# Kernel tuning notes

Measured on AMD Instinct MI355X. Metric: run time of the kernel, lower is better.

## Reference

```python
import jax, jax.numpy as jnp
import numpy as np

D = 4       # number of TT dimensions
N = 128     # mode size per dimension (Ns)
R = 16      # TT rank (RMAX)
B = 262144  # batch of query points


def setup_inputs() -> dict:
    key = jax.random.key(0)
    ks = jax.random.split(key, 5)
    # points in [-1, 1] (remap_needed=True assumes this domain)
    x = jax.random.uniform(ks[0], (B, D), dtype=jnp.float32) * 2.0 - 1.0
    core0 = jax.random.normal(ks[1], (1, N, R), dtype=jnp.float32)
    core1 = jax.random.normal(ks[2], (R, N, R), dtype=jnp.float32)
    core2 = jax.random.normal(ks[3], (R, N, R), dtype=jnp.float32)
    core3 = jax.random.normal(ks[4], (R, N, 1), dtype=jnp.float32)
    return {"x": x, "core0": core0, "core1": core1, "core2": core2, "core3": core3}


def _forward(x, cores):
    # remap: (x + 1) / 2 * (Ns[0] - 1)  (module uses Ns[0] for all dims)
    n0 = cores[0].shape[1]
    xr = (x + 1.0) * 0.5 * (n0 - 1)
    # per-dim clamp to [0, Ns[i]-1]
    ns = jnp.array([c.shape[1] for c in cores], dtype=x.dtype)  # [D]
    xc = jnp.clip(xr, 0.0, ns - 1.0)  # broadcast over D
    idx_low = jnp.floor(xc).astype(jnp.int32)   # [B, D]
    idx_high = jnp.ceil(xc).astype(jnp.int32)   # [B, D]
    wh = xc - idx_low.astype(x.dtype)           # [B, D] interpolation weights
    # gather + linear interpolation per core -> list of [r_prev, B, r_next]
    newcores = []
    for i, c in enumerate(cores):
        lo = jnp.take(c, idx_low[:, i], axis=1)   # [r_prev, B, r_next]
        hi = jnp.take(c, idx_high[:, i], axis=1)  # [r_prev, B, r_next]
        w = wh[:, i][None, :, None]               # [1, B, 1]
        newcores.append((1.0 - w) * lo + w * hi)
    # chained batched contraction, right to left (matches ttcontract)
    res = newcores[-1]
    for i in range(len(newcores) - 2, 0, -1):
        res = jnp.einsum('abc,cbk->abk', newcores[i], res)
    return jnp.einsum('abc,cbk->b', newcores[0], res)  # [B]


def reference(x, core0, core1, core2, core3):
    return _forward(x, [core0, core1, core2, core3])
```

## Files before the change

kernel.cpp:

```cpp
#include <hip/hip_runtime.h>
#include <hip/hip_bf16.h>

typedef unsigned int uint32;
typedef unsigned short u16;

#define NPT 128
#define RNK 16
#define MIDROW 264
#define MIDROW_U32 132
#define EDGEROW 20
#define SMEM_BYTES (2*NPT*MIDROW*2 + 2*NPT*EDGEROW*4)

#if defined(__has_builtin)
#if __has_builtin(__builtin_amdgcn_fdot2_f32_bf16)
#define HAVE_BFDOT2 1
#endif
#endif

__device__ __forceinline__ float bl(uint32 u){ return __uint_as_float(u << 16); }
__device__ __forceinline__ float bh(uint32 u){ return __uint_as_float(u & 0xffff0000u); }

#ifdef HAVE_BFDOT2
typedef __bf16 v2bf __attribute__((ext_vector_type(2)));
__device__ __forceinline__ v2bf bc(uint32 u){ return __builtin_bit_cast(v2bf, u); }

__device__ __forceinline__ float dot16b(const uint32* vp, uint4 U0, uint4 U1) {
  float s0 = 0.f, s1 = 0.f;
  s0 = __builtin_amdgcn_fdot2_f32_bf16(bc(vp[0]), bc(U0.x), s0, false);
  s0 = __builtin_amdgcn_fdot2_f32_bf16(bc(vp[1]), bc(U0.y), s0, false);
  s0 = __builtin_amdgcn_fdot2_f32_bf16(bc(vp[2]), bc(U0.z), s0, false);
  s0 = __builtin_amdgcn_fdot2_f32_bf16(bc(vp[3]), bc(U0.w), s0, false);
  s1 = __builtin_amdgcn_fdot2_f32_bf16(bc(vp[4]), bc(U1.x), s1, false);
  s1 = __builtin_amdgcn_fdot2_f32_bf16(bc(vp[5]), bc(U1.y), s1, false);
  s1 = __builtin_amdgcn_fdot2_f32_bf16(bc(vp[6]), bc(U1.z), s1, false);
  s1 = __builtin_amdgcn_fdot2_f32_bf16(bc(vp[7]), bc(U1.w), s1, false);
  return s0 + s1;
}
#else
__device__ __forceinline__ float dot16(const float* v, uint4 U0, uint4 U1) {
  float s0 = fmaf(v[1],  bh(U0.x), v[0]*bl(U0.x));
  s0 = fmaf(v[2],  bl(U0.y), s0); s0 = fmaf(v[3],  bh(U0.y), s0);
  float s1 = fmaf(v[5],  bh(U0.z), v[4]*bl(U0.z));
  s1 = fmaf(v[6],  bl(U0.w), s1); s1 = fmaf(v[7],  bh(U0.w), s1);
  float s2 = fmaf(v[9],  bh(U1.x), v[8]*bl(U1.x));
  s2 = fmaf(v[10], bl(U1.y), s2); s2 = fmaf(v[11], bh(U1.y), s2);
  float s3 = fmaf(v[13], bh(U1.z), v[12]*bl(U1.z));
  s3 = fmaf(v[14], bl(U1.w), s3); s3 = fmaf(v[15], bh(U1.w), s3);
  return (s0 + s1) + (s2 + s3);
}
#endif

__device__ __forceinline__ void tt_mid(const uint32* __restrict__ base, float xc, float v[16]) {
  int n0 = (int)xc;
  float w = xc - (float)n0;
  int n1 = min(n0 + 1, NPT - 1);
  const uint32* r0 = base + n0 * MIDROW_U32;
  const uint32* r1 = base + n1 * MIDROW_U32;

#ifdef HAVE_BFDOT2
  uint32 vp[8];
#pragma unroll
  for (int k = 0; k < 8; ++k) {
    __hip_bfloat16 l = __float2bfloat16(v[2*k]);
    __hip_bfloat16 h = __float2bfloat16(v[2*k+1]);
    vp[k] = (uint32)(*(u16*)&l) | ((uint32)(*(u16*)&h) << 16);
  }
#endif

  float nv[16];
#pragma unroll
  for (int j = 0; j < 16; ++j) {
    const uint4* p0 = (const uint4*)(r0 + j * 8);
    const uint4* p1 = (const uint4*)(r1 + j * 8);
    uint4 A0 = p0[0], A1 = p0[1];
    uint4 B0 = p1[0], B1 = p1[1];
#ifdef HAVE_BFDOT2
    float a = dot16b(vp, A0, A1);
    float b = dot16b(vp, B0, B1);
#else
    float a = dot16(v, A0, A1);
    float b = dot16(v, B0, B1);
#endif
    nv[j] = fmaf(w, b - a, a);
  }
#pragma unroll
  for (int j = 0; j < 16; ++j) v[j] = nv[j];
}

__device__ __forceinline__ float remap_clamp(float x) {
  float xr = (x + 1.0f) * 0.5f * (float)(NPT - 1);
  return fminf(fmaxf(xr, 0.0f), (float)(NPT - 1));
}

__global__ __launch_bounds__(1024, 4) void tt_kernel(
    const float* __restrict__ x,  const float* __restrict__ g0,
    const float* __restrict__ g1, const float* __restrict__ g2,
    const float* __restrict__ g3, float* __restrict__ out, int npts)
{
  extern __shared__ char smem[];
  unsigned short* c1 = (unsigned short*)smem;
  unsigned short* c2 = c1 + NPT * MIDROW;
  float* c0 = (float*)(c2 + NPT * MIDROW);
  float* c3 = c0 + NPT * EDGEROW;

  for (int t = threadIdx.x; t < RNK * NPT * RNK; t += blockDim.x) {
    int i = t >> 11;
    int n = (t >> 4) & (NPT - 1);
    int j = t & (RNK - 1);
    __hip_bfloat16 h1 = __float2bfloat16(g1[t]);
    __hip_bfloat16 h2 = __float2bfloat16(g2[t]);
    c1[n * MIDROW + j * 16 + i] = *(u16*)&h1;
    c2[n * MIDROW + j * 16 + i] = *(u16*)&h2;
  }
  for (int t = threadIdx.x; t < NPT * RNK; t += blockDim.x) {
    int n = t >> 4;
    int i = t & (RNK - 1);
    c0[n * EDGEROW + i] = g0[t];
    c3[n * EDGEROW + i] = g3[i * NPT + n];
  }
  __syncthreads();

  int p = blockIdx.x * blockDim.x + threadIdx.x;
  if (p >= npts) return;
  float4 xv = reinterpret_cast<const float4*>(x)[p];

  float v[16];
  {
    float xc = remap_clamp(xv.x);
    int n0 = (int)xc; float w = xc - (float)n0; int n1 = min(n0 + 1, NPT - 1);
    const float4* L = (const float4*)(c0 + n0 * EDGEROW);
    const float4* H = (const float4*)(c0 + n1 * EDGEROW);
#pragma unroll
    for (int k = 0; k < 4; ++k) {
      float4 l = L[k], h = H[k];
      v[4*k+0] = fmaf(w, h.x - l.x, l.x);
      v[4*k+1] = fmaf(w, h.y - l.y, l.y);
      v[4*k+2] = fmaf(w, h.z - l.z, l.z);
      v[4*k+3] = fmaf(w, h.w - l.w, l.w);
    }
  }
  tt_mid((const uint32*)c1, remap_clamp(xv.y), v);
  tt_mid((const uint32*)c2, remap_clamp(xv.z), v);
  float acc;
  {
    float xc = remap_clamp(xv.w);
    int n0 = (int)xc; float w = xc - (float)n0; int n1 = min(n0 + 1, NPT - 1);
    const float4* L = (const float4*)(c3 + n0 * EDGEROW);
    const float4* H = (const float4*)(c3 + n1 * EDGEROW);
    float a0 = 0.f, a1 = 0.f, a2 = 0.f, a3 = 0.f;
#pragma unroll
    for (int k = 0; k < 4; ++k) {
      float4 l = L[k], h = H[k];
      a0 = fmaf(v[4*k+0], fmaf(w, h.x - l.x, l.x), a0);
      a1 = fmaf(v[4*k+1], fmaf(w, h.y - l.y, l.y), a1);
      a2 = fmaf(v[4*k+2], fmaf(w, h.z - l.z, l.z), a2);
      a3 = fmaf(v[4*k+3], fmaf(w, h.w - l.w, l.w), a3);
    }
    acc = (a0 + a1) + (a2 + a3);
  }
  out[p] = acc;
}

extern "C" void kernel_launch(void* const* d_in, const int* in_sizes, int n_in,
                              void* d_out, int out_size, void* d_ws, size_t ws_size,
                              hipStream_t stream) {
  const float* x  = (const float*)d_in[0];
  const float* g0 = (const float*)d_in[1];
  const float* g1 = (const float*)d_in[2];
  const float* g2 = (const float*)d_in[3];
  const float* g3 = (const float*)d_in[4];
  float* out = (float*)d_out;

  int B = in_sizes[0] / 4;
  hipFuncSetAttribute(reinterpret_cast<const void*>(tt_kernel),
                      hipFuncAttributeMaxDynamicSharedMemorySize, SMEM_BYTES);
  int block = 1024;
  int grid = (B + block - 1) / block;
  tt_kernel<<<grid, block, SMEM_BYTES, stream>>>(x, g0, g1, g2, g3, out, B);
}
```

Measured before the change: 83.48 us.

## Split each point across two lanes and reuse one shared buffer for mid cores

```diff
diff --git a/kernel.cpp b/kernel.cpp
--- a/kernel.cpp
+++ b/kernel.cpp
@@ -8,8 +8,8 @@
 #define RNK 16
 #define MIDROW 264
 #define MIDROW_U32 132
-#define EDGEROW 20
-#define SMEM_BYTES (2*NPT*MIDROW*2 + 2*NPT*EDGEROW*4)
+#define EROW 24
+#define SMEM_BYTES (NPT*MIDROW*2 + 2*NPT*EROW*2)
 
 #if defined(__has_builtin)
 #if __has_builtin(__builtin_amdgcn_fdot2_f32_bf16)
@@ -19,6 +19,12 @@
 
 __device__ __forceinline__ float bl(uint32 u){ return __uint_as_float(u << 16); }
 __device__ __forceinline__ float bh(uint32 u){ return __uint_as_float(u & 0xffff0000u); }
+
+__device__ __forceinline__ uint32 pk2(float a, float b){
+  __hip_bfloat16 l = __float2bfloat16(a);
+  __hip_bfloat16 h = __float2bfloat16(b);
+  return (uint32)(*(u16*)&l) | ((uint32)(*(u16*)&h) << 16);
+}
 
 #ifdef HAVE_BFDOT2
 typedef __bf16 v2bf __attribute__((ext_vector_type(2)));
@@ -50,41 +56,32 @@
 }
 #endif
 
-__device__ __forceinline__ void tt_mid(const uint32* __restrict__ base, float xc, float v[16]) {
-  int n0 = (int)xc;
-  float w = xc - (float)n0;
-  int n1 = min(n0 + 1, NPT - 1);
-  const uint32* r0 = base + n0 * MIDROW_U32;
-  const uint32* r1 = base + n1 * MIDROW_U32;
-
-#ifdef HAVE_BFDOT2
-  uint32 vp[8];
-#pragma unroll
-  for (int k = 0; k < 8; ++k) {
-    __hip_bfloat16 l = __float2bfloat16(v[2*k]);
-    __hip_bfloat16 h = __float2bfloat16(v[2*k+1]);
-    vp[k] = (uint32)(*(u16*)&l) | ((uint32)(*(u16*)&h) << 16);
-  }
-#endif
-
-  float nv[16];
-#pragma unroll
-  for (int j = 0; j < 16; ++j) {
-    const uint4* p0 = (const uint4*)(r0 + j * 8);
-    const uint4* p1 = (const uint4*)(r1 + j * 8);
-    uint4 A0 = p0[0], A1 = p0[1];
-    uint4 B0 = p1[0], B1 = p1[1];
-#ifdef HAVE_BFDOT2
-    float a = dot16b(vp, A0, A1);
-    float b = dot16b(vp, B0, B1);
-#else
-    float a = dot16(v, A0, A1);
-    float b = dot16(v, B0, B1);
-#endif
-    nv[j] = fmaf(w, b - a, a);
-  }
-#pragma unroll
-  for (int j = 0; j < 16; ++j) v[j] = nv[j];
+__device__ __forceinline__ void lerp8(uint4 lo, uint4 hi, float w, float* o) {
+  o[0] = fmaf(w, bl(hi.x) - bl(lo.x), bl(lo.x));
+  o[1] = fmaf(w, bh(hi.x) - bh(lo.x), bh(lo.x));
+  o[2] = fmaf(w, bl(hi.y) - bl(lo.y), bl(lo.y));
+  o[3] = fmaf(w, bh(hi.y) - bh(lo.y), bh(lo.y));
+  o[4] = fmaf(w, bl(hi.z) - bl(lo.z), bl(lo.z));
+  o[5] = fmaf(w, bh(hi.z) - bh(lo.z), bh(lo.z));
+  o[6] = fmaf(w, bl(hi.w) - bl(lo.w), bl(lo.w));
+  o[7] = fmaf(w, bh(hi.w) - bh(lo.w), bh(lo.w));
+}
+
+__device__ __forceinline__ void stage_mid(const float* __restrict__ g, u16* dst) {
+#pragma unroll
+  for (int c = 0; c < 4; ++c) {
+    int t = (int)threadIdx.x + c * 1024;
+    int n = t >> 5;
+    int j = (t >> 1) & 15;
+    int h = t & 1;
+    const float* s = g + h * 8 * 2048 + n * 16 + j;
+    uint4 wv;
+    wv.x = pk2(s[0],        s[2048]);
+    wv.y = pk2(s[2 * 2048], s[3 * 2048]);
+    wv.z = pk2(s[4 * 2048], s[5 * 2048]);
+    wv.w = pk2(s[6 * 2048], s[7 * 2048]);
+    *(uint4*)(dst + n * MIDROW + j * 16 + h * 8) = wv;
+  }
 }
 
 __device__ __forceinline__ float remap_clamp(float x) {
@@ -92,73 +89,131 @@
   return fminf(fmaxf(xr, 0.0f), (float)(NPT - 1));
 }
 
-__global__ __launch_bounds__(1024, 4) void tt_kernel(
+__global__ __launch_bounds__(1024, 8) void tt_kernel(
     const float* __restrict__ x,  const float* __restrict__ g0,
     const float* __restrict__ g1, const float* __restrict__ g2,
     const float* __restrict__ g3, float* __restrict__ out, int npts)
 {
   extern __shared__ char smem[];
-  unsigned short* c1 = (unsigned short*)smem;
-  unsigned short* c2 = c1 + NPT * MIDROW;
-  float* c0 = (float*)(c2 + NPT * MIDROW);
-  float* c3 = c0 + NPT * EDGEROW;
-
-  for (int t = threadIdx.x; t < RNK * NPT * RNK; t += blockDim.x) {
-    int i = t >> 11;
-    int n = (t >> 4) & (NPT - 1);
-    int j = t & (RNK - 1);
-    __hip_bfloat16 h1 = __float2bfloat16(g1[t]);
-    __hip_bfloat16 h2 = __float2bfloat16(g2[t]);
-    c1[n * MIDROW + j * 16 + i] = *(u16*)&h1;
-    c2[n * MIDROW + j * 16 + i] = *(u16*)&h2;
-  }
-  for (int t = threadIdx.x; t < NPT * RNK; t += blockDim.x) {
-    int n = t >> 4;
-    int i = t & (RNK - 1);
-    c0[n * EDGEROW + i] = g0[t];
-    c3[n * EDGEROW + i] = g3[i * NPT + n];
+  u16* mid = (u16*)smem;
+  u16* e0  = mid + NPT * MIDROW;
+  u16* e3  = e0 + NPT * EROW;
+
+  stage_mid(g1, mid);
+  if (threadIdx.x < 512) {
+    int t = (int)threadIdx.x;
+    if (t < 256) {
+      int n = t >> 1, h = t & 1;
+      const float4* s = (const float4*)(g0 + n * 16 + h * 8);
+      float4 a = s[0], b = s[1];
+      uint4 wv = make_uint4(pk2(a.x, a.y), pk2(a.z, a.w), pk2(b.x, b.y), pk2(b.z, b.w));
+      *(uint4*)(e0 + n * EROW + h * 8) = wv;
+    } else {
+      t -= 256;
+      int n = t >> 1, h = t & 1;
+      const float* s = g3 + h * 8 * NPT + n;
+      uint4 wv = make_uint4(pk2(s[0],       s[NPT]),     pk2(s[2 * NPT], s[3 * NPT]),
+                            pk2(s[4 * NPT], s[5 * NPT]), pk2(s[6 * NPT], s[7 * NPT]));
+      *(uint4*)(e3 + n * EROW + h * 8) = wv;
+    }
   }
   __syncthreads();
 
-  int p = blockIdx.x * blockDim.x + threadIdx.x;
-  if (p >= npts) return;
-  float4 xv = reinterpret_cast<const float4*>(x)[p];
+  const int lane = (int)threadIdx.x & 63;
+  const int wid  = (int)threadIdx.x >> 6;
+  const int half = lane >> 5;
+  const int p    = (int)blockIdx.x * 512 + wid * 32 + (lane & 31);
+  const bool active = p < npts;
+  float4 xv = active ? reinterpret_cast<const float4*>(x)[p]
+                     : make_float4(-1.f, -1.f, -1.f, -1.f);
 
   float v[16];
   {
     float xc = remap_clamp(xv.x);
     int n0 = (int)xc; float w = xc - (float)n0; int n1 = min(n0 + 1, NPT - 1);
-    const float4* L = (const float4*)(c0 + n0 * EDGEROW);
-    const float4* H = (const float4*)(c0 + n1 * EDGEROW);
-#pragma unroll
-    for (int k = 0; k < 4; ++k) {
-      float4 l = L[k], h = H[k];
-      v[4*k+0] = fmaf(w, h.x - l.x, l.x);
-      v[4*k+1] = fmaf(w, h.y - l.y, l.y);
-      v[4*k+2] = fmaf(w, h.z - l.z, l.z);
-      v[4*k+3] = fmaf(w, h.w - l.w, l.w);
+    const uint4* L = (const uint4*)(e0 + n0 * EROW);
+    const uint4* H = (const uint4*)(e0 + n1 * EROW);
+    uint4 l0 = L[0], l1 = L[1], h0 = H[0], h1 = H[1];
+    lerp8(l0, h0, w, v);
+    lerp8(l1, h1, w, v + 8);
+  }
+
+  float nv[8];
+  {
+#ifdef HAVE_BFDOT2
+    uint32 vp[8];
+#pragma unroll
+    for (int k = 0; k < 8; ++k) vp[k] = pk2(v[2 * k], v[2 * k + 1]);
+#endif
+    float xc = remap_clamp(xv.y);
+    int n0 = (int)xc; float w = xc - (float)n0; int n1 = min(n0 + 1, NPT - 1);
+    const uint32* r0 = (const uint32*)mid + n0 * MIDROW_U32 + (half << 6);
+    const uint32* r1 = (const uint32*)mid + n1 * MIDROW_U32 + (half << 6);
+#pragma unroll
+    for (int jj = 0; jj < 8; ++jj) {
+      const uint4* p0 = (const uint4*)(r0 + jj * 8);
+      const uint4* p1 = (const uint4*)(r1 + jj * 8);
+      uint4 A0 = p0[0], A1 = p0[1], B0 = p1[0], B1 = p1[1];
+#ifdef HAVE_BFDOT2
+      float a = dot16b(vp, A0, A1);
+      float b = dot16b(vp, B0, B1);
+#else
+      float a = dot16(v, A0, A1);
+      float b = dot16(v, B0, B1);
+#endif
+      nv[jj] = fmaf(w, b - a, a);
     }
   }
-  tt_mid((const uint32*)c1, remap_clamp(xv.y), v);
-  tt_mid((const uint32*)c2, remap_clamp(xv.z), v);
-  float acc;
+#pragma unroll
+  for (int k = 0; k < 8; ++k) {
+    float ov = __shfl_xor(nv[k], 32, 64);
+    v[k]     = half ? ov    : nv[k];
+    v[8 + k] = half ? nv[k] : ov;
+  }
+
+  __syncthreads();
+  stage_mid(g2, mid);
+  __syncthreads();
+
+  {
+#ifdef HAVE_BFDOT2
+    uint32 vp[8];
+#pragma unroll
+    for (int k = 0; k < 8; ++k) vp[k] = pk2(v[2 * k], v[2 * k + 1]);
+#endif
+    float xc = remap_clamp(xv.z);
+    int n0 = (int)xc; float w = xc - (float)n0; int n1 = min(n0 + 1, NPT - 1);
+    const uint32* r0 = (const uint32*)mid + n0 * MIDROW_U32 + (half << 6);
+    const uint32* r1 = (const uint32*)mid + n1 * MIDROW_U32 + (half << 6);
+#pragma unroll
+    for (int jj = 0; jj < 8; ++jj) {
+      const uint4* p0 = (const uint4*)(r0 + jj * 8);
+      const uint4* p1 = (const uint4*)(r1 + jj * 8);
+      uint4 A0 = p0[0], A1 = p0[1], B0 = p1[0], B1 = p1[1];
+#ifdef HAVE_BFDOT2
+      float a = dot16b(vp, A0, A1);
+      float b = dot16b(vp, B0, B1);
+#else
+      float a = dot16(v, A0, A1);
+      float b = dot16(v, B0, B1);
+#endif
+      nv[jj] = fmaf(w, b - a, a);
+    }
+  }
+
+  float acc = 0.f;
   {
     float xc = remap_clamp(xv.w);
     int n0 = (int)xc; float w = xc - (float)n0; int n1 = min(n0 + 1, NPT - 1);
-    const float4* L = (const float4*)(c3 + n0 * EDGEROW);
-    const float4* H = (const float4*)(c3 + n1 * EDGEROW);
-    float a0 = 0.f, a1 = 0.f, a2 = 0.f, a3 = 0.f;
-#pragma unroll
-    for (int k = 0; k < 4; ++k) {
-      float4 l = L[k], h = H[k];
-      a0 = fmaf(v[4*k+0], fmaf(w, h.x - l.x, l.x), a0);
-      a1 = fmaf(v[4*k+1], fmaf(w, h.y - l.y, l.y), a1);
-      a2 = fmaf(v[4*k+2], fmaf(w, h.z - l.z, l.z), a2);
-      a3 = fmaf(v[4*k+3], fmaf(w, h.w - l.w, l.w), a3);
-    }
-    acc = (a0 + a1) + (a2 + a3);
-  }
-  out[p] = acc;
+    uint4 lo = *(const uint4*)(e3 + n0 * EROW + half * 8);
+    uint4 hi = *(const uint4*)(e3 + n1 * EROW + half * 8);
+    float c3v[8];
+    lerp8(lo, hi, w, c3v);
+#pragma unroll
+    for (int k = 0; k < 8; ++k) acc = fmaf(nv[k], c3v[k], acc);
+  }
+  acc += __shfl_xor(acc, 32, 64);
+  if (active && half == 0) out[p] = acc;
 }
 
 extern "C" void kernel_launch(void* const* d_in, const int* in_sizes, int n_in,
@@ -175,6 +230,6 @@
   hipFuncSetAttribute(reinterpret_cast<const void*>(tt_kernel),
                       hipFuncAttributeMaxDynamicSharedMemorySize, SMEM_BYTES);
   int block = 1024;
-  int grid = (B + block - 1) / block;
+  int grid = (2 * B + block - 1) / block;
   tt_kernel<<<grid, block, SMEM_BYTES, stream>>>(x, g0, g1, g2, g3, out, B);
 }
```

Measured after the change: 85.75 us. +2.7%, slower.

## Precompute bf16 LDS image once, stream cores via global_load_lds, reuse single mid buffer

Applied to the files above, without the earlier changes.

```diff
diff --git a/kernel.cpp b/kernel.cpp
--- a/kernel.cpp
+++ b/kernel.cpp
@@ -8,8 +8,20 @@
 #define RNK 16
 #define MIDROW 264
 #define MIDROW_U32 132
-#define EDGEROW 20
-#define SMEM_BYTES (2*NPT*MIDROW*2 + 2*NPT*EDGEROW*4)
+#define EROW 24
+
+#define MID_ELEMS (NPT*MIDROW)
+#define EDGE_ELEMS (NPT*EROW)
+#define IMG_C1 0
+#define IMG_E0 33792
+#define IMG_E3 36864
+#define IMG_C2 39936
+#define IMG_TOTAL 73728
+#define WS_BYTES (IMG_TOTAL*2)
+
+#define SMEM_BYTES (MID_ELEMS*2 + 2*EDGE_ELEMS*2)
+#define PHASE0_CHUNKS (SMEM_BYTES/1024)
+#define PHASE1_CHUNKS (MID_ELEMS*2/1024)
 
 #if defined(__has_builtin)
 #if __has_builtin(__builtin_amdgcn_fdot2_f32_bf16)
@@ -19,6 +31,12 @@
 
 __device__ __forceinline__ float bl(uint32 u){ return __uint_as_float(u << 16); }
 __device__ __forceinline__ float bh(uint32 u){ return __uint_as_float(u & 0xffff0000u); }
+
+__device__ __forceinline__ uint32 pk2(float a, float b){
+  __hip_bfloat16 l = __float2bfloat16(a);
+  __hip_bfloat16 h = __float2bfloat16(b);
+  return (uint32)(*(u16*)&l) | ((uint32)(*(u16*)&h) << 16);
+}
 
 #ifdef HAVE_BFDOT2
 typedef __bf16 v2bf __attribute__((ext_vector_type(2)));
@@ -50,6 +68,22 @@
 }
 #endif
 
+__device__ __forceinline__ void lerp8(uint4 lo, uint4 hi, float w, float* o) {
+  o[0] = fmaf(w, bl(hi.x) - bl(lo.x), bl(lo.x));
+  o[1] = fmaf(w, bh(hi.x) - bh(lo.x), bh(lo.x));
+  o[2] = fmaf(w, bl(hi.y) - bl(lo.y), bl(lo.y));
+  o[3] = fmaf(w, bh(hi.y) - bh(lo.y), bh(lo.y));
+  o[4] = fmaf(w, bl(hi.z) - bl(lo.z), bl(lo.z));
+  o[5] = fmaf(w, bh(hi.z) - bh(lo.z), bh(lo.z));
+  o[6] = fmaf(w, bl(hi.w) - bl(lo.w), bl(lo.w));
+  o[7] = fmaf(w, bh(hi.w) - bh(lo.w), bh(lo.w));
+}
+
+__device__ __forceinline__ float remap_clamp(float x) {
+  float xr = (x + 1.0f) * 0.5f * (float)(NPT - 1);
+  return fminf(fmaxf(xr, 0.0f), (float)(NPT - 1));
+}
+
 __device__ __forceinline__ void tt_mid(const uint32* __restrict__ base, float xc, float v[16]) {
   int n0 = (int)xc;
   float w = xc - (float)n0;
@@ -60,11 +94,7 @@
 #ifdef HAVE_BFDOT2
   uint32 vp[8];
 #pragma unroll
-  for (int k = 0; k < 8; ++k) {
-    __hip_bfloat16 l = __float2bfloat16(v[2*k]);
-    __hip_bfloat16 h = __float2bfloat16(v[2*k+1]);
-    vp[k] = (uint32)(*(u16*)&l) | ((uint32)(*(u16*)&h) << 16);
-  }
+  for (int k = 0; k < 8; ++k) vp[k] = pk2(v[2*k], v[2*k+1]);
 #endif
 
   float nv[16];
@@ -87,78 +117,123 @@
   for (int j = 0; j < 16; ++j) v[j] = nv[j];
 }
 
-__device__ __forceinline__ float remap_clamp(float x) {
-  float xr = (x + 1.0f) * 0.5f * (float)(NPT - 1);
-  return fminf(fmaxf(xr, 0.0f), (float)(NPT - 1));
-}
-
-__global__ __launch_bounds__(1024, 4) void tt_kernel(
+__global__ __launch_bounds__(256) void prep_kernel(
+    const float* __restrict__ g0, const float* __restrict__ g1,
+    const float* __restrict__ g2, const float* __restrict__ g3,
+    u16* __restrict__ img)
+{
+  int t = (int)blockIdx.x * 256 + (int)threadIdx.x;
+  if (t >= IMG_TOTAL) return;
+  float val = 0.f;
+  if (t < IMG_E0) {
+    int n = t / MIDROW, r = t % MIDROW;
+    if (r < 256) { int j = r >> 4, i = r & 15; val = g1[i * 2048 + n * 16 + j]; }
+  } else if (t < IMG_E3) {
+    int e = t - IMG_E0; int n = e / EROW, r = e % EROW;
+    if (r < 16) val = g0[n * 16 + r];
+  } else if (t < IMG_C2) {
+    int e = t - IMG_E3; int n = e / EROW, r = e % EROW;
+    if (r < 16) val = g3[r * NPT + n];
+  } else {
+    int e = t - IMG_C2; int n = e / MIDROW, r = e % MIDROW;
+    if (r < 256) { int j = r >> 4, i = r & 15; val = g2[i * 2048 + n * 16 + j]; }
+  }
+  __hip_bfloat16 h = __float2bfloat16(val);
+  img[t] = *(u16*)&h;
+}
+
+__device__ __forceinline__ void gload16(const u16* g, u16* l) {
+  __builtin_amdgcn_global_load_lds(
+      (const __attribute__((address_space(1))) uint32*)g,
+      (__attribute__((address_space(3))) uint32*)l, 16, 0, 0);
+}
+
+__global__ __launch_bounds__(512, 4) void tt_kernel(
     const float* __restrict__ x,  const float* __restrict__ g0,
     const float* __restrict__ g1, const float* __restrict__ g2,
-    const float* __restrict__ g3, float* __restrict__ out, int npts)
+    const float* __restrict__ g3, const u16* __restrict__ img,
+    float* __restrict__ out, int npts)
 {
   extern __shared__ char smem[];
-  unsigned short* c1 = (unsigned short*)smem;
-  unsigned short* c2 = c1 + NPT * MIDROW;
-  float* c0 = (float*)(c2 + NPT * MIDROW);
-  float* c3 = c0 + NPT * EDGEROW;
-
-  for (int t = threadIdx.x; t < RNK * NPT * RNK; t += blockDim.x) {
-    int i = t >> 11;
-    int n = (t >> 4) & (NPT - 1);
-    int j = t & (RNK - 1);
-    __hip_bfloat16 h1 = __float2bfloat16(g1[t]);
-    __hip_bfloat16 h2 = __float2bfloat16(g2[t]);
-    c1[n * MIDROW + j * 16 + i] = *(u16*)&h1;
-    c2[n * MIDROW + j * 16 + i] = *(u16*)&h2;
-  }
-  for (int t = threadIdx.x; t < NPT * RNK; t += blockDim.x) {
-    int n = t >> 4;
-    int i = t & (RNK - 1);
-    c0[n * EDGEROW + i] = g0[t];
-    c3[n * EDGEROW + i] = g3[i * NPT + n];
+  u16* mid = (u16*)smem;
+  u16* e0  = mid + MID_ELEMS;
+  u16* e3  = e0 + EDGE_ELEMS;
+
+  const int lane = (int)threadIdx.x & 63;
+  const int wid  = (int)threadIdx.x >> 6;
+
+  if (img) {
+    for (int c = wid; c < PHASE0_CHUNKS; c += 8)
+      gload16(img + c * 512 + lane * 8, mid + c * 512 + lane * 8);
+  } else {
+    for (int t = (int)threadIdx.x; t < RNK * NPT * RNK; t += 512) {
+      int i = t >> 11, n = (t >> 4) & (NPT - 1), j = t & 15;
+      __hip_bfloat16 h = __float2bfloat16(g1[t]);
+      mid[n * MIDROW + j * 16 + i] = *(u16*)&h;
+    }
+    for (int t = (int)threadIdx.x; t < NPT * RNK; t += 512) {
+      int n = t >> 4, i = t & 15;
+      __hip_bfloat16 a = __float2bfloat16(g0[t]);
+      __hip_bfloat16 b = __float2bfloat16(g3[i * NPT + n]);
+      e0[n * EROW + i] = *(u16*)&a;
+      e3[n * EROW + i] = *(u16*)&b;
+    }
   }
   __syncthreads();
 
-  int p = blockIdx.x * blockDim.x + threadIdx.x;
-  if (p >= npts) return;
-  float4 xv = reinterpret_cast<const float4*>(x)[p];
+  const int p = (int)blockIdx.x * 512 + (int)threadIdx.x;
+  const bool active = p < npts;
+  float4 xv = active ? reinterpret_cast<const float4*>(x)[p]
+                     : make_float4(-1.f, -1.f, -1.f, -1.f);
 
   float v[16];
   {
     float xc = remap_clamp(xv.x);
     int n0 = (int)xc; float w = xc - (float)n0; int n1 = min(n0 + 1, NPT - 1);
-    const float4* L = (const float4*)(c0 + n0 * EDGEROW);
-    const float4* H = (const float4*)(c0 + n1 * EDGEROW);
-#pragma unroll
-    for (int k = 0; k < 4; ++k) {
-      float4 l = L[k], h = H[k];
-      v[4*k+0] = fmaf(w, h.x - l.x, l.x);
-      v[4*k+1] = fmaf(w, h.y - l.y, l.y);
-      v[4*k+2] = fmaf(w, h.z - l.z, l.z);
-      v[4*k+3] = fmaf(w, h.w - l.w, l.w);
-    }
-  }
-  tt_mid((const uint32*)c1, remap_clamp(xv.y), v);
-  tt_mid((const uint32*)c2, remap_clamp(xv.z), v);
-  float acc;
+    const uint4* L = (const uint4*)(e0 + n0 * EROW);
+    const uint4* H = (const uint4*)(e0 + n1 * EROW);
+    uint4 l0 = L[0], l1 = L[1], h0 = H[0], h1 = H[1];
+    lerp8(l0, h0, w, v);
+    lerp8(l1, h1, w, v + 8);
+  }
+
+  tt_mid((const uint32*)mid, remap_clamp(xv.y), v);
+
+  __syncthreads();
+  if (img) {
+    for (int c = wid; c < PHASE1_CHUNKS; c += 8)
+      gload16(img + IMG_C2 + c * 512 + lane * 8, mid + c * 512 + lane * 8);
+  } else {
+    for (int t = (int)threadIdx.x; t < RNK * NPT * RNK; t += 512) {
+      int i = t >> 11, n = (t >> 4) & (NPT - 1), j = t & 15;
+      __hip_bfloat16 h = __float2bfloat16(g2[t]);
+      mid[n * MIDROW + j * 16 + i] = *(u16*)&h;
+    }
+  }
+  __syncthreads();
+
+  tt_mid((const uint32*)mid, remap_clamp(xv.z), v);
+
+  float acc = 0.f;
   {
     float xc = remap_clamp(xv.w);
     int n0 = (int)xc; float w = xc - (float)n0; int n1 = min(n0 + 1, NPT - 1);
-    const float4* L = (const float4*)(c3 + n0 * EDGEROW);
-    const float4* H = (const float4*)(c3 + n1 * EDGEROW);
+    const uint4* L = (const uint4*)(e3 + n0 * EROW);
+    const uint4* H = (const uint4*)(e3 + n1 * EROW);
+    float c3v[16];
+    lerp8(L[0], H[0], w, c3v);
+    lerp8(L[1], H[1], w, c3v + 8);
     float a0 = 0.f, a1 = 0.f, a2 = 0.f, a3 = 0.f;
 #pragma unroll
     for (int k = 0; k < 4; ++k) {
-      float4 l = L[k], h = H[k];
-      a0 = fmaf(v[4*k+0], fmaf(w, h.x - l.x, l.x), a0);
-      a1 = fmaf(v[4*k+1], fmaf(w, h.y - l.y, l.y), a1);
-      a2 = fmaf(v[4*k+2], fmaf(w, h.z - l.z, l.z), a2);
-      a3 = fmaf(v[4*k+3], fmaf(w, h.w - l.w, l.w), a3);
+      a0 = fmaf(v[4*k+0], c3v[4*k+0], a0);
+      a1 = fmaf(v[4*k+1], c3v[4*k+1], a1);
+      a2 = fmaf(v[4*k+2], c3v[4*k+2], a2);
+      a3 = fmaf(v[4*k+3], c3v[4*k+3], a3);
     }
     acc = (a0 + a1) + (a2 + a3);
   }
-  out[p] = acc;
+  if (active) out[p] = acc;
 }
 
 extern "C" void kernel_launch(void* const* d_in, const int* in_sizes, int n_in,
@@ -172,9 +247,16 @@
   float* out = (float*)d_out;
 
   int B = in_sizes[0] / 4;
+  bool useimg = (d_ws != nullptr) && (ws_size >= (size_t)WS_BYTES);
+  u16* img = useimg ? (u16*)d_ws : nullptr;
+
+  if (useimg) {
+    prep_kernel<<<(IMG_TOTAL + 255) / 256, 256, 0, stream>>>(g0, g1, g2, g3, img);
+  }
+
   hipFuncSetAttribute(reinterpret_cast<const void*>(tt_kernel),
                       hipFuncAttributeMaxDynamicSharedMemorySize, SMEM_BYTES);
-  int block = 1024;
+  int block = 512;
   int grid = (B + block - 1) / block;
-  tt_kernel<<<grid, block, SMEM_BYTES, stream>>>(x, g0, g1, g2, g3, out, B);
-}
+  tt_kernel<<<grid, block, SMEM_BYTES, stream>>>(x, g0, g1, g2, g3, img, out, B);
+}
```

Result: slower. 125.9 us (+50.8%).

## Prebuild bf16 core image once and stream it into LDS asynchronously

Applied to the files above, without the earlier changes.

```diff
diff --git a/kernel.cpp b/kernel.cpp
--- a/kernel.cpp
+++ b/kernel.cpp
@@ -8,8 +8,14 @@
 #define RNK 16
 #define MIDROW 264
 #define MIDROW_U32 132
-#define EDGEROW 20
-#define SMEM_BYTES (2*NPT*MIDROW*2 + 2*NPT*EDGEROW*4)
+#define EROW 20
+
+#define OFF_E   67584
+#define OFF_C2  88064
+#define WS_BYTES 155648
+#define SMEM_BYTES WS_BYTES
+#define P0_CHUNKS (OFF_C2 / 1024)
+#define P1_CHUNKS ((WS_BYTES - OFF_C2) / 1024)
 
 #if defined(__has_builtin)
 #if __has_builtin(__builtin_amdgcn_fdot2_f32_bf16)
@@ -19,6 +25,12 @@
 
 __device__ __forceinline__ float bl(uint32 u){ return __uint_as_float(u << 16); }
 __device__ __forceinline__ float bh(uint32 u){ return __uint_as_float(u & 0xffff0000u); }
+
+__device__ __forceinline__ uint32 pk2(float a, float b){
+  __hip_bfloat16 l = __float2bfloat16(a);
+  __hip_bfloat16 h = __float2bfloat16(b);
+  return (uint32)(*(u16*)&l) | ((uint32)(*(u16*)&h) << 16);
+}
 
 #ifdef HAVE_BFDOT2
 typedef __bf16 v2bf __attribute__((ext_vector_type(2)));
@@ -50,6 +62,11 @@
 }
 #endif
 
+__device__ __forceinline__ float remap_clamp(float x) {
+  float xr = (x + 1.0f) * 0.5f * (float)(NPT - 1);
+  return fminf(fmaxf(xr, 0.0f), (float)(NPT - 1));
+}
+
 __device__ __forceinline__ void tt_mid(const uint32* __restrict__ base, float xc, float v[16]) {
   int n0 = (int)xc;
   float w = xc - (float)n0;
@@ -60,11 +77,7 @@
 #ifdef HAVE_BFDOT2
   uint32 vp[8];
 #pragma unroll
-  for (int k = 0; k < 8; ++k) {
-    __hip_bfloat16 l = __float2bfloat16(v[2*k]);
-    __hip_bfloat16 h = __float2bfloat16(v[2*k+1]);
-    vp[k] = (uint32)(*(u16*)&l) | ((uint32)(*(u16*)&h) << 16);
-  }
+  for (int k = 0; k < 8; ++k) vp[k] = pk2(v[2*k], v[2*k+1]);
 #endif
 
   float nv[16];
@@ -87,49 +100,91 @@
   for (int j = 0; j < 16; ++j) v[j] = nv[j];
 }
 
-__device__ __forceinline__ float remap_clamp(float x) {
-  float xr = (x + 1.0f) * 0.5f * (float)(NPT - 1);
-  return fminf(fmaxf(xr, 0.0f), (float)(NPT - 1));
+__global__ __launch_bounds__(256) void prep_kernel(
+    const float* __restrict__ g0, const float* __restrict__ g1,
+    const float* __restrict__ g2, const float* __restrict__ g3,
+    char* __restrict__ img)
+{
+  int t = (int)blockIdx.x * 256 + (int)threadIdx.x;
+  if (t < 67584) {
+    int h = t >= 33792;
+    int e = h ? t - 33792 : t;
+    int n = e / MIDROW, r = e % MIDROW;
+    float val = 0.f;
+    if (r < 256) { int j = r >> 4, i = r & 15; val = (h ? g2 : g1)[i * 2048 + n * 16 + j]; }
+    __hip_bfloat16 b = __float2bfloat16(val);
+    ((u16*)img)[h ? (OFF_C2 / 2 + e) : e] = *(u16*)&b;
+  } else if (t < 72704) {
+    int e = t - 67584;
+    int h = e >= 2560;
+    int q = h ? e - 2560 : e;
+    int n = q / EROW, k = q % EROW;
+    float val = 0.f;
+    if (k < 16) val = h ? g3[k * NPT + n] : g0[n * 16 + k];
+    ((float*)(img + OFF_E))[e] = val;
+  }
+}
+
+__device__ __forceinline__ void gload16(const char* g, char* l) {
+  __builtin_amdgcn_global_load_lds(
+      (const __attribute__((address_space(1))) uint32*)g,
+      (__attribute__((address_space(3))) uint32*)l, 16, 0, 0);
 }
 
 __global__ __launch_bounds__(1024, 4) void tt_kernel(
     const float* __restrict__ x,  const float* __restrict__ g0,
     const float* __restrict__ g1, const float* __restrict__ g2,
-    const float* __restrict__ g3, float* __restrict__ out, int npts)
+    const float* __restrict__ g3, const char* __restrict__ img,
+    float* __restrict__ out, int npts)
 {
   extern __shared__ char smem[];
-  unsigned short* c1 = (unsigned short*)smem;
-  unsigned short* c2 = c1 + NPT * MIDROW;
-  float* c0 = (float*)(c2 + NPT * MIDROW);
-  float* c3 = c0 + NPT * EDGEROW;
-
-  for (int t = threadIdx.x; t < RNK * NPT * RNK; t += blockDim.x) {
-    int i = t >> 11;
-    int n = (t >> 4) & (NPT - 1);
-    int j = t & (RNK - 1);
-    __hip_bfloat16 h1 = __float2bfloat16(g1[t]);
-    __hip_bfloat16 h2 = __float2bfloat16(g2[t]);
-    c1[n * MIDROW + j * 16 + i] = *(u16*)&h1;
-    c2[n * MIDROW + j * 16 + i] = *(u16*)&h2;
-  }
-  for (int t = threadIdx.x; t < NPT * RNK; t += blockDim.x) {
-    int n = t >> 4;
-    int i = t & (RNK - 1);
-    c0[n * EDGEROW + i] = g0[t];
-    c3[n * EDGEROW + i] = g3[i * NPT + n];
+  u16* c1   = (u16*)smem;
+  float* e0 = (float*)(smem + OFF_E);
+  float* e3 = e0 + NPT * EROW;
+  u16* c2   = (u16*)(smem + OFF_C2);
+
+  const int lane = (int)threadIdx.x & 63;
+  const int wid  = (int)threadIdx.x >> 6;
+
+  if (img) {
+    for (int c = wid; c < P0_CHUNKS; c += 16)
+      gload16(img + c * 1024 + lane * 16, smem + c * 1024 + lane * 16);
+  } else {
+    for (int t = (int)threadIdx.x; t < RNK * NPT * RNK; t += 1024) {
+      int i = t >> 11, n = (t >> 4) & (NPT - 1), j = t & 15;
+      __hip_bfloat16 h = __float2bfloat16(g1[t]);
+      c1[n * MIDROW + j * 16 + i] = *(u16*)&h;
+    }
+    for (int t = (int)threadIdx.x; t < NPT * RNK; t += 1024) {
+      int n = t >> 4, i = t & 15;
+      e0[n * EROW + i] = g0[t];
+      e3[n * EROW + i] = g3[i * NPT + n];
+    }
   }
   __syncthreads();
 
-  int p = blockIdx.x * blockDim.x + threadIdx.x;
-  if (p >= npts) return;
-  float4 xv = reinterpret_cast<const float4*>(x)[p];
+  if (img) {
+    for (int c = wid; c < P1_CHUNKS; c += 16)
+      gload16(img + OFF_C2 + c * 1024 + lane * 16, smem + OFF_C2 + c * 1024 + lane * 16);
+  } else {
+    for (int t = (int)threadIdx.x; t < RNK * NPT * RNK; t += 1024) {
+      int i = t >> 11, n = (t >> 4) & (NPT - 1), j = t & 15;
+      __hip_bfloat16 h = __float2bfloat16(g2[t]);
+      c2[n * MIDROW + j * 16 + i] = *(u16*)&h;
+    }
+  }
+
+  const int p = (int)blockIdx.x * 1024 + (int)threadIdx.x;
+  const bool active = p < npts;
+  float4 xv = active ? reinterpret_cast<const float4*>(x)[p]
+                     : make_float4(-1.f, -1.f, -1.f, -1.f);
 
   float v[16];
   {
     float xc = remap_clamp(xv.x);
     int n0 = (int)xc; float w = xc - (float)n0; int n1 = min(n0 + 1, NPT - 1);
-    const float4* L = (const float4*)(c0 + n0 * EDGEROW);
-    const float4* H = (const float4*)(c0 + n1 * EDGEROW);
+    const float4* L = (const float4*)(e0 + n0 * EROW);
+    const float4* H = (const float4*)(e0 + n1 * EROW);
 #pragma unroll
     for (int k = 0; k < 4; ++k) {
       float4 l = L[k], h = H[k];
@@ -139,14 +194,19 @@
       v[4*k+3] = fmaf(w, h.w - l.w, l.w);
     }
   }
+
   tt_mid((const uint32*)c1, remap_clamp(xv.y), v);
+
+  __syncthreads();
+
   tt_mid((const uint32*)c2, remap_clamp(xv.z), v);
+
   float acc;
   {
     float xc = remap_clamp(xv.w);
     int n0 = (int)xc; float w = xc - (float)n0; int n1 = min(n0 + 1, NPT - 1);
-    const float4* L = (const float4*)(c3 + n0 * EDGEROW);
-    const float4* H = (const float4*)(c3 + n1 * EDGEROW);
+    const float4* L = (const float4*)(e3 + n0 * EROW);
+    const float4* H = (const float4*)(e3 + n1 * EROW);
     float a0 = 0.f, a1 = 0.f, a2 = 0.f, a3 = 0.f;
 #pragma unroll
     for (int k = 0; k < 4; ++k) {
@@ -158,7 +218,7 @@
     }
     acc = (a0 + a1) + (a2 + a3);
   }
-  out[p] = acc;
+  if (active) out[p] = acc;
 }
 
 extern "C" void kernel_launch(void* const* d_in, const int* in_sizes, int n_in,
@@ -172,9 +232,16 @@
   float* out = (float*)d_out;
 
   int B = in_sizes[0] / 4;
+  bool useimg = (d_ws != nullptr) && (ws_size >= (size_t)WS_BYTES);
+  char* img = useimg ? (char*)d_ws : nullptr;
+
+  if (useimg) {
+    prep_kernel<<<(72704 + 255) / 256, 256, 0, stream>>>(g0, g1, g2, g3, img);
+  }
+
   hipFuncSetAttribute(reinterpret_cast<const void*>(tt_kernel),
                       hipFuncAttributeMaxDynamicSharedMemorySize, SMEM_BYTES);
   int block = 1024;
   int grid = (B + block - 1) / block;
-  tt_kernel<<<grid, block, SMEM_BYTES, stream>>>(x, g0, g1, g2, g3, out, B);
-}
+  tt_kernel<<<grid, block, SMEM_BYTES, stream>>>(x, g0, g1, g2, g3, img, out, B);
+}
```

New measurement: 124.3 us. 48.9% more time.
